# Performance work log

Hardware: AMD Instinct MI355X
Metric: run time of the kernel (lower is better)

Reference implementation:

```python
import jax, jax.numpy as jnp
import numpy as np

K, D, N, T, B = 8, 16, 32, 200, 2048
_LOG2PI = float(np.log(2.0 * np.pi))


def setup_inputs() -> dict:
    key = jax.random.key(0)
    ks = jax.random.split(key, 13)
    return {
        "discrete_states": jax.random.randint(ks[0], (B, T), 0, K),
        "continuous_states": jax.random.normal(ks[1], (B, T, D), dtype=jnp.float32),
        "obs": jax.random.normal(ks[2], (B, T, N), dtype=jnp.float32),
        "discrete_init_logits": jax.random.normal(ks[3], (K,), dtype=jnp.float32),
        "continuous_init_locs": jax.random.normal(ks[4], (K, D), dtype=jnp.float32),
        "continuous_init_log_scales": jax.random.normal(ks[5], (K, D), dtype=jnp.float32),
        "state_transition_logits": jax.random.normal(ks[6], (K, K), dtype=jnp.float32),
        "dynamics_matrices": jax.random.normal(ks[7], (K, D, D), dtype=jnp.float32) * 0.3,
        "dynamics_offsets": jax.random.normal(ks[8], (K, D), dtype=jnp.float32),
        # NOTE: original code uses dynamics_log_scales directly as a scale (missing .exp());
        # we keep that math faithfully but init it strictly positive to stay finite.
        "dynamics_log_scales": jax.random.uniform(ks[9], (K, D), minval=0.5, maxval=1.5, dtype=jnp.float32),
        "emission_matrices": jax.random.normal(ks[10], (K, N, D), dtype=jnp.float32),
        "emission_offsets": jax.random.normal(ks[11], (K, N), dtype=jnp.float32),
        "emission_log_scales": jax.random.normal(ks[12], (K, N), dtype=jnp.float32),
    }


def _normal_lp(x, loc, scale):
    # elementwise Normal log-prob
    return -0.5 * jnp.square((x - loc) / scale) - jnp.log(scale) - 0.5 * _LOG2PI


def reference(discrete_states, continuous_states, obs,
              discrete_init_logits, continuous_init_locs, continuous_init_log_scales,
              state_transition_logits, dynamics_matrices, dynamics_offsets,
              dynamics_log_scales, emission_matrices, emission_offsets,
              emission_log_scales):
    """log p(s_{1:T}, z_{1:T}, x_{1:T}) -> [B]"""
    s0 = discrete_states[:, 0]                      # [B]
    z0 = continuous_states[:, 0]                    # [B,D]
    # p(s_1)
    lp = jax.nn.log_softmax(discrete_init_logits)[s0]
    # p(z_1 | s_1)
    lp = lp + _normal_lp(z0, continuous_init_locs[s0],
                         jnp.exp(continuous_init_log_scales[s0])).sum(-1)
    # p(s_t | s_{t-1}) for t=2..T, fully vectorized over time
    s_prev = discrete_states[:, :-1]
    s_cur = discrete_states[:, 1:]
    trans = jax.nn.log_softmax(state_transition_logits, axis=-1)  # [K,K]
    lp = lp + trans[s_prev, s_cur].sum(-1)
    # p(z_t | z_{t-1}, s_t)
    A = dynamics_matrices[s_cur]                    # [B,T-1,D,D] gather
    dyn_loc = jnp.einsum('btij,btj->bti', A, continuous_states[:, :-1]) + dynamics_offsets[s_cur]
    dyn_scale = dynamics_log_scales[s_cur]          # faithful: original omits .exp()
    lp = lp + _normal_lp(continuous_states[:, 1:], dyn_loc, dyn_scale).sum((-1, -2))
    # p(x_t | z_t, s_t) for all t
    C = emission_matrices[discrete_states]          # [B,T,N,D] gather
    em_loc = jnp.einsum('btij,btj->bti', C, continuous_states) + emission_offsets[discrete_states]
    em_scale = jnp.exp(emission_log_scales[discrete_states])
    lp = lp + _normal_lp(obs, em_loc, em_scale).sum((-1, -2))
    return lp
```

## Files before the change

kernel.cpp:

```cpp
#include <hip/hip_runtime.h>

#define KK 8
#define DD 16
#define NN 32
#define TT 200
#define BB 2048

#define SC 516
#define SA 260
#define SE 36
#define SD 20

__device__ __forceinline__ float dot16(const float* __restrict__ row,
                                       const float* __restrict__ z) {
  const float4* r4 = reinterpret_cast<const float4*>(row);
  float4 c0 = r4[0], c1 = r4[1], c2 = r4[2], c3 = r4[3];
  float a = c0.x * z[0], b = c0.y * z[1];
  a = fmaf(c0.z, z[2], a);  b = fmaf(c0.w, z[3], b);
  a = fmaf(c1.x, z[4], a);  b = fmaf(c1.y, z[5], b);
  a = fmaf(c1.z, z[6], a);  b = fmaf(c1.w, z[7], b);
  a = fmaf(c2.x, z[8], a);  b = fmaf(c2.y, z[9], b);
  a = fmaf(c2.z, z[10], a); b = fmaf(c2.w, z[11], b);
  a = fmaf(c3.x, z[12], a); b = fmaf(c3.y, z[13], b);
  a = fmaf(c3.z, z[14], a); b = fmaf(c3.w, z[15], b);
  return a + b;
}

__device__ __forceinline__ void load16(float* __restrict__ d,
                                       const float* __restrict__ s) {
  const float4* p = reinterpret_cast<const float4*>(s);
  float4 a0 = p[0], a1 = p[1], a2 = p[2], a3 = p[3];
  d[0] = a0.x;  d[1] = a0.y;  d[2] = a0.z;  d[3] = a0.w;
  d[4] = a1.x;  d[5] = a1.y;  d[6] = a1.z;  d[7] = a1.w;
  d[8] = a2.x;  d[9] = a2.y;  d[10] = a2.z; d[11] = a2.w;
  d[12] = a3.x; d[13] = a3.y; d[14] = a3.z; d[15] = a3.w;
}

__global__ __launch_bounds__(256) void slds_lp_kernel(
    const int* __restrict__ dsts,
    const float* __restrict__ zg,
    const float* __restrict__ obsg,
    const float* __restrict__ initlg,
    const float* __restrict__ initloc,
    const float* __restrict__ initls,
    const float* __restrict__ transg,
    const float* __restrict__ Ag,
    const float* __restrict__ dynoff,
    const float* __restrict__ dynls,
    const float* __restrict__ Cg,
    const float* __restrict__ emoff,
    const float* __restrict__ emls,
    float* __restrict__ out)
{
  __shared__ __align__(16) float sC[KK * SC];
  __shared__ __align__(16) float sA[KK * SA];
  __shared__ __align__(16) float sEmOff[KK * SE];
  __shared__ __align__(16) float sEmInv[KK * SE];
  __shared__ __align__(16) float sDynOff[KK * SD];
  __shared__ __align__(16) float sDynInv[KK * SD];
  __shared__ __align__(16) float sInitLoc[KK * SD];
  __shared__ __align__(16) float sInitInv[KK * SD];
  __shared__ float sTrans[KK * KK];
  __shared__ float sEmConst[KK];
  __shared__ float sDynConst[KK];
  __shared__ float sInitLp[KK];

  const float HALF_LOG2PI = 0.91893853320467274178f;
  const int tid = threadIdx.x;

  for (int i = tid; i < KK * NN * DD; i += 256) {
    int k = i >> 9, r = i & 511;
    sC[k * SC + r] = Cg[i];
  }
  for (int i = tid; i < KK * DD * DD; i += 256) {
    int k = i >> 8, r = i & 255;
    sA[k * SA + r] = Ag[i];
  }
  if (tid < KK * NN) {
    int k = tid >> 5, n = tid & 31;
    sEmOff[k * SE + n] = emoff[tid];
    sEmInv[k * SE + n] = expf(-emls[tid]);
  }
  if (tid < KK * DD) {
    int k = tid >> 4, d = tid & 15;
    sDynOff[k * SD + d] = dynoff[tid];
    sDynInv[k * SD + d] = 1.0f / dynls[tid];
    sInitLoc[k * SD + d] = initloc[tid];
    sInitInv[k * SD + d] = expf(-initls[tid]);
  }
  if (tid < KK * KK) {
    int kr = tid >> 3;
    float mx = transg[kr * KK];
    for (int j = 1; j < KK; ++j) mx = fmaxf(mx, transg[kr * KK + j]);
    float ss = 0.f;
    for (int j = 0; j < KK; ++j) ss += expf(transg[kr * KK + j] - mx);
    sTrans[tid] = transg[tid] - (logf(ss) + mx);
  }
  if (tid < KK) {
    int k = tid;
    float se = 0.f;
    for (int n = 0; n < NN; ++n) se -= emls[k * NN + n];
    sEmConst[k] = se - NN * HALF_LOG2PI;
    float sd = 0.f;
    for (int d = 0; d < DD; ++d) sd -= logf(dynls[k * DD + d]);
    sDynConst[k] = sd - DD * HALF_LOG2PI;
    float mx = initlg[0];
    for (int j = 1; j < KK; ++j) mx = fmaxf(mx, initlg[j]);
    float ss = 0.f;
    for (int j = 0; j < KK; ++j) ss += expf(initlg[j] - mx);
    float si = 0.f;
    for (int d = 0; d < DD; ++d) si -= initls[k * DD + d];
    sInitLp[k] = initlg[k] - (logf(ss) + mx) + si - DD * HALF_LOG2PI;
  }
  __syncthreads();

  const int base = blockIdx.x * 320;
  for (int ofs = tid; ofs < 320; ofs += 256) {
    const int item = base + ofs;
    const int b = item / TT;
    const int t = item - b * TT;

    float z[16];
    load16(z, zg + (size_t)item * DD);
    const int s = dsts[item];

    const float4* o4 = reinterpret_cast<const float4*>(obsg + (size_t)item * NN);
    const int cb = s * SC;
    const int eb4 = s * (SE / 4);
    float acc = 0.f;
#pragma unroll 1
    for (int g = 0; g < 8; ++g) {
      float4 o = o4[g];
      float4 off = reinterpret_cast<const float4*>(sEmOff)[eb4 + g];
      float4 inv = reinterpret_cast<const float4*>(sEmInv)[eb4 + g];
      int n0 = g * 4;
      float l0 = dot16(&sC[cb + (n0 + 0) * DD], z) + off.x;
      float l1 = dot16(&sC[cb + (n0 + 1) * DD], z) + off.y;
      float l2 = dot16(&sC[cb + (n0 + 2) * DD], z) + off.z;
      float l3 = dot16(&sC[cb + (n0 + 3) * DD], z) + off.w;
      float d0 = (o.x - l0) * inv.x;
      float d1 = (o.y - l1) * inv.y;
      float d2 = (o.z - l2) * inv.z;
      float d3 = (o.w - l3) * inv.w;
      acc = fmaf(d0, d0, acc); acc = fmaf(d1, d1, acc);
      acc = fmaf(d2, d2, acc); acc = fmaf(d3, d3, acc);
    }
    float lp = -0.5f * acc + sEmConst[s];

    if (t != 0) {
      const int sp = dsts[item - 1];
      float zp[16];
      load16(zp, zg + (size_t)(item - 1) * DD);
      const int ab = s * SA;
      const int db4 = s * (SD / 4);
      float a2acc = 0.f;
#pragma unroll
      for (int g = 0; g < 4; ++g) {
        const int i0 = g * 4;
        float4 off = reinterpret_cast<const float4*>(sDynOff)[db4 + g];
        float4 inv = reinterpret_cast<const float4*>(sDynInv)[db4 + g];
        float l0 = dot16(&sA[ab + (i0 + 0) * DD], zp) + off.x;
        float l1 = dot16(&sA[ab + (i0 + 1) * DD], zp) + off.y;
        float l2 = dot16(&sA[ab + (i0 + 2) * DD], zp) + off.z;
        float l3 = dot16(&sA[ab + (i0 + 3) * DD], zp) + off.w;
        float d0 = (z[i0 + 0] - l0) * inv.x;
        float d1 = (z[i0 + 1] - l1) * inv.y;
        float d2 = (z[i0 + 2] - l2) * inv.z;
        float d3 = (z[i0 + 3] - l3) * inv.w;
        a2acc = fmaf(d0, d0, a2acc); a2acc = fmaf(d1, d1, a2acc);
        a2acc = fmaf(d2, d2, a2acc); a2acc = fmaf(d3, d3, a2acc);
      }
      lp += -0.5f * a2acc + sDynConst[s] + sTrans[sp * KK + s];
    } else {
      const int ib4 = s * (SD / 4);
      float a2acc = 0.f;
#pragma unroll
      for (int g = 0; g < 4; ++g) {
        const int i0 = g * 4;
        float4 loc = reinterpret_cast<const float4*>(sInitLoc)[ib4 + g];
        float4 inv = reinterpret_cast<const float4*>(sInitInv)[ib4 + g];
        float d0 = (z[i0 + 0] - loc.x) * inv.x;
        float d1 = (z[i0 + 1] - loc.y) * inv.y;
        float d2 = (z[i0 + 2] - loc.z) * inv.z;
        float d3 = (z[i0 + 3] - loc.w) * inv.w;
        a2acc = fmaf(d0, d0, a2acc); a2acc = fmaf(d1, d1, a2acc);
        a2acc = fmaf(d2, d2, a2acc); a2acc = fmaf(d3, d3, a2acc);
      }
      lp += -0.5f * a2acc + sInitLp[s];
    }

    const int lane = tid & 63;
    float v = lp;
#pragma unroll
    for (int off = 1; off < 64; off <<= 1) {
      float ov = __shfl_up(v, off, 64);
      int obk = __shfl_up(b, off, 64);
      if (lane >= off && obk == b) v += ov;
    }
    int nb = __shfl_down(b, 1, 64);
    if (lane == 63 || nb != b) atomicAdd(&out[b], v);
  }
}

extern "C" void kernel_launch(void* const* d_in, const int* in_sizes, int n_in,
                              void* d_out, int out_size, void* d_ws, size_t ws_size,
                              hipStream_t stream) {
  const int*   dsts    = (const int*)d_in[0];
  const float* zg      = (const float*)d_in[1];
  const float* obsg    = (const float*)d_in[2];
  const float* initlg  = (const float*)d_in[3];
  const float* initloc = (const float*)d_in[4];
  const float* initls  = (const float*)d_in[5];
  const float* transg  = (const float*)d_in[6];
  const float* Ag      = (const float*)d_in[7];
  const float* dynoff  = (const float*)d_in[8];
  const float* dynls   = (const float*)d_in[9];
  const float* Cg      = (const float*)d_in[10];
  const float* emoff   = (const float*)d_in[11];
  const float* emls    = (const float*)d_in[12];
  float* out = (float*)d_out;

  hipMemsetAsync(d_out, 0, BB * sizeof(float), stream);

  slds_lp_kernel<<<1280, 256, 0, stream>>>(dsts, zg, obsg, initlg, initloc,
                                           initls, transg, Ag, dynoff, dynls,
                                           Cg, emoff, emls, out);
}
```

Baseline: 142.5 us.

## Drop dynamics and init tables from LDS and give each block more items

The per-block staging of the dynamics matrices and the init loc/scale tables into shared memory is removed. Those values are now read directly from global memory through the cache, and the init inverse scales are computed with expf inline. The kernel now launches fewer blocks that each process 400 items, which spreads the shared-memory prologue over more work and lowers LDS use per block. The emission loop moves after the dynamics term, and the atomic flush also fires at the last item because a wave is now only partly active. The tradeoff is uncoalesced global/L1 reads of A per thread, in place of LDS reads.

```diff
diff --git a/kernel.cpp b/kernel.cpp
--- a/kernel.cpp
+++ b/kernel.cpp
@@ -7,7 +7,6 @@
 #define BB 2048
 
 #define SC 516
-#define SA 260
 #define SE 36
 #define SD 20
 
@@ -53,13 +52,10 @@
     float* __restrict__ out)
 {
   __shared__ __align__(16) float sC[KK * SC];
-  __shared__ __align__(16) float sA[KK * SA];
   __shared__ __align__(16) float sEmOff[KK * SE];
   __shared__ __align__(16) float sEmInv[KK * SE];
   __shared__ __align__(16) float sDynOff[KK * SD];
   __shared__ __align__(16) float sDynInv[KK * SD];
-  __shared__ __align__(16) float sInitLoc[KK * SD];
-  __shared__ __align__(16) float sInitInv[KK * SD];
   __shared__ float sTrans[KK * KK];
   __shared__ float sEmConst[KK];
   __shared__ float sDynConst[KK];
@@ -72,10 +68,6 @@
     int k = i >> 9, r = i & 511;
     sC[k * SC + r] = Cg[i];
   }
-  for (int i = tid; i < KK * DD * DD; i += 256) {
-    int k = i >> 8, r = i & 255;
-    sA[k * SA + r] = Ag[i];
-  }
   if (tid < KK * NN) {
     int k = tid >> 5, n = tid & 31;
     sEmOff[k * SE + n] = emoff[tid];
@@ -85,8 +77,6 @@
     int k = tid >> 4, d = tid & 15;
     sDynOff[k * SD + d] = dynoff[tid];
     sDynInv[k * SD + d] = 1.0f / dynls[tid];
-    sInitLoc[k * SD + d] = initloc[tid];
-    sInitInv[k * SD + d] = expf(-initls[tid]);
   }
   if (tid < KK * KK) {
     int kr = tid >> 3;
@@ -114,8 +104,8 @@
   }
   __syncthreads();
 
-  const int base = blockIdx.x * 320;
-  for (int ofs = tid; ofs < 320; ofs += 256) {
+  const int base = blockIdx.x * 400;
+  for (int ofs = tid; ofs < 400; ofs += 256) {
     const int item = base + ofs;
     const int b = item / TT;
     const int t = item - b * TT;
@@ -123,35 +113,13 @@
     float z[16];
     load16(z, zg + (size_t)item * DD);
     const int s = dsts[item];
-
-    const float4* o4 = reinterpret_cast<const float4*>(obsg + (size_t)item * NN);
-    const int cb = s * SC;
-    const int eb4 = s * (SE / 4);
-    float acc = 0.f;
-#pragma unroll 1
-    for (int g = 0; g < 8; ++g) {
-      float4 o = o4[g];
-      float4 off = reinterpret_cast<const float4*>(sEmOff)[eb4 + g];
-      float4 inv = reinterpret_cast<const float4*>(sEmInv)[eb4 + g];
-      int n0 = g * 4;
-      float l0 = dot16(&sC[cb + (n0 + 0) * DD], z) + off.x;
-      float l1 = dot16(&sC[cb + (n0 + 1) * DD], z) + off.y;
-      float l2 = dot16(&sC[cb + (n0 + 2) * DD], z) + off.z;
-      float l3 = dot16(&sC[cb + (n0 + 3) * DD], z) + off.w;
-      float d0 = (o.x - l0) * inv.x;
-      float d1 = (o.y - l1) * inv.y;
-      float d2 = (o.z - l2) * inv.z;
-      float d3 = (o.w - l3) * inv.w;
-      acc = fmaf(d0, d0, acc); acc = fmaf(d1, d1, acc);
-      acc = fmaf(d2, d2, acc); acc = fmaf(d3, d3, acc);
-    }
-    float lp = -0.5f * acc + sEmConst[s];
+    float lp;
 
     if (t != 0) {
       const int sp = dsts[item - 1];
       float zp[16];
       load16(zp, zg + (size_t)(item - 1) * DD);
-      const int ab = s * SA;
+      const float* __restrict__ Ab = Ag + (size_t)s * (DD * DD);
       const int db4 = s * (SD / 4);
       float a2acc = 0.f;
 #pragma unroll
@@ -159,10 +127,10 @@
         const int i0 = g * 4;
         float4 off = reinterpret_cast<const float4*>(sDynOff)[db4 + g];
         float4 inv = reinterpret_cast<const float4*>(sDynInv)[db4 + g];
-        float l0 = dot16(&sA[ab + (i0 + 0) * DD], zp) + off.x;
-        float l1 = dot16(&sA[ab + (i0 + 1) * DD], zp) + off.y;
-        float l2 = dot16(&sA[ab + (i0 + 2) * DD], zp) + off.z;
-        float l3 = dot16(&sA[ab + (i0 + 3) * DD], zp) + off.w;
+        float l0 = dot16(&Ab[(i0 + 0) * DD], zp) + off.x;
+        float l1 = dot16(&Ab[(i0 + 1) * DD], zp) + off.y;
+        float l2 = dot16(&Ab[(i0 + 2) * DD], zp) + off.z;
+        float l3 = dot16(&Ab[(i0 + 3) * DD], zp) + off.w;
         float d0 = (z[i0 + 0] - l0) * inv.x;
         float d1 = (z[i0 + 1] - l1) * inv.y;
         float d2 = (z[i0 + 2] - l2) * inv.z;
@@ -170,23 +138,49 @@
         a2acc = fmaf(d0, d0, a2acc); a2acc = fmaf(d1, d1, a2acc);
         a2acc = fmaf(d2, d2, a2acc); a2acc = fmaf(d3, d3, a2acc);
       }
-      lp += -0.5f * a2acc + sDynConst[s] + sTrans[sp * KK + s];
+      lp = -0.5f * a2acc + sDynConst[s] + sTrans[sp * KK + s];
     } else {
-      const int ib4 = s * (SD / 4);
+      const float* __restrict__ ploc = initloc + s * DD;
+      const float* __restrict__ pls  = initls + s * DD;
       float a2acc = 0.f;
 #pragma unroll
       for (int g = 0; g < 4; ++g) {
         const int i0 = g * 4;
-        float4 loc = reinterpret_cast<const float4*>(sInitLoc)[ib4 + g];
-        float4 inv = reinterpret_cast<const float4*>(sInitInv)[ib4 + g];
-        float d0 = (z[i0 + 0] - loc.x) * inv.x;
-        float d1 = (z[i0 + 1] - loc.y) * inv.y;
-        float d2 = (z[i0 + 2] - loc.z) * inv.z;
-        float d3 = (z[i0 + 3] - loc.w) * inv.w;
+        float4 loc = reinterpret_cast<const float4*>(ploc)[g];
+        float4 ls  = reinterpret_cast<const float4*>(pls)[g];
+        float d0 = (z[i0 + 0] - loc.x) * expf(-ls.x);
+        float d1 = (z[i0 + 1] - loc.y) * expf(-ls.y);
+        float d2 = (z[i0 + 2] - loc.z) * expf(-ls.z);
+        float d3 = (z[i0 + 3] - loc.w) * expf(-ls.w);
         a2acc = fmaf(d0, d0, a2acc); a2acc = fmaf(d1, d1, a2acc);
         a2acc = fmaf(d2, d2, a2acc); a2acc = fmaf(d3, d3, a2acc);
       }
-      lp += -0.5f * a2acc + sInitLp[s];
+      lp = -0.5f * a2acc + sInitLp[s];
+    }
+
+    {
+      const float4* o4 = reinterpret_cast<const float4*>(obsg + (size_t)item * NN);
+      const int cb = s * SC;
+      const int eb4 = s * (SE / 4);
+      float acc = 0.f;
+#pragma unroll 1
+      for (int g = 0; g < 8; ++g) {
+        float4 o = o4[g];
+        float4 off = reinterpret_cast<const float4*>(sEmOff)[eb4 + g];
+        float4 inv = reinterpret_cast<const float4*>(sEmInv)[eb4 + g];
+        int n0 = g * 4;
+        float l0 = dot16(&sC[cb + (n0 + 0) * DD], z) + off.x;
+        float l1 = dot16(&sC[cb + (n0 + 1) * DD], z) + off.y;
+        float l2 = dot16(&sC[cb + (n0 + 2) * DD], z) + off.z;
+        float l3 = dot16(&sC[cb + (n0 + 3) * DD], z) + off.w;
+        float d0 = (o.x - l0) * inv.x;
+        float d1 = (o.y - l1) * inv.y;
+        float d2 = (o.z - l2) * inv.z;
+        float d3 = (o.w - l3) * inv.w;
+        acc = fmaf(d0, d0, acc); acc = fmaf(d1, d1, acc);
+        acc = fmaf(d2, d2, acc); acc = fmaf(d3, d3, acc);
+      }
+      lp += -0.5f * acc + sEmConst[s];
     }
 
     const int lane = tid & 63;
@@ -198,7 +192,7 @@
       if (lane >= off && obk == b) v += ov;
     }
     int nb = __shfl_down(b, 1, 64);
-    if (lane == 63 || nb != b) atomicAdd(&out[b], v);
+    if (lane == 63 || ofs == 399 || nb != b) atomicAdd(&out[b], v);
   }
 }
 
@@ -222,7 +216,7 @@
 
   hipMemsetAsync(d_out, 0, BB * sizeof(float), stream);
 
-  slds_lp_kernel<<<1280, 256, 0, stream>>>(dsts, zg, obsg, initlg, initloc,
+  slds_lp_kernel<<<1024, 256, 0, stream>>>(dsts, zg, obsg, initlg, initloc,
                                            initls, transg, Ag, dynoff, dynls,
                                            Cg, emoff, emls, out);
 }
```

Measured after the change: 177.5 us. 24.5% more time.
